# Optimization experiments

Hardware: AMD Instinct MI355X
Metric: run time of the kernel (lower is better)

## Reference

```python
import jax, jax.numpy as jnp
import numpy as np

NEG_BIG = -1e30  # safe "-inf" for masked softmax (avoids NaN for fully-masked rows)


def setup_inputs() -> dict:
    key = jax.random.key(0)
    k1, k2, k3, k4, k5, k6 = jax.random.split(key, 6)
    B, Kmax, D, C = 64, 512, 256, 1000
    deep_feats = jax.random.normal(k1, (B, D), dtype=jnp.float32)
    n = jax.random.normal(k2, (B, Kmax, D), dtype=jnp.float32)
    w = jax.random.uniform(k3, (B, Kmax), dtype=jnp.float32)
    cls_score = jax.random.normal(k4, (B, Kmax, C), dtype=jnp.float32)
    target = jax.random.randint(k5, (B,), 0, C, dtype=jnp.int64)
    lengths = jax.random.randint(k6, (B,), 1, Kmax + 1, dtype=jnp.int64)
    return {"deep_feats": deep_feats, "n": n, "w": w, "cls_score": cls_score,
            "target": target, "lengths": lengths}


def reference(deep_feats, n, w, cls_score, target, lengths):
    # deep_feats: [B,D], n: [B,Kmax,D], w: [B,Kmax], cls_score: [B,Kmax,C]
    # target: [B] int, lengths: [B] int (number of valid neighbors per sample)
    B, Kmax, C = cls_score.shape
    mask = jnp.arange(Kmax)[None, :] < lengths[:, None]          # [B,Kmax]

    # per-neighbor L2 distance ||f_i - n_ij||
    diff = deep_feats[:, None, :] - n                             # [B,Kmax,D]
    dist = jnp.sqrt(jnp.sum(diff * diff, axis=-1))                # [B,Kmax]

    s = -w * dist                                                 # [B,Kmax]
    # f_loss = sum_i -w_i . dist_i over valid neighbors
    f_loss = jnp.sum(jnp.where(mask, s, 0.0))

    # rho_i = softmax over valid neighbors of -w*dist
    logits = jnp.where(mask, s, NEG_BIG)
    rho = jax.nn.softmax(logits, axis=-1) * mask                  # [B,Kmax]

    # per-neighbor cross-entropy: -log_softmax(cls_score[b,k])[target[b]]
    logp = jax.nn.log_softmax(cls_score, axis=-1)                 # [B,Kmax,C]
    idx = jnp.broadcast_to(target[:, None, None], (B, Kmax, 1))
    ce = -jnp.take_along_axis(logp, idx, axis=-1)[..., 0]         # [B,Kmax]

    g_loss = jnp.sum(rho * ce)
    return f_loss + g_loss
```

## Files before the change

### kernel.cpp

```cpp
#include <hip/hip_runtime.h>
#include <math.h>

#define BB 64
#define KMAX 512
#define DD 256
#define CC 1000
#define NBLK1 (BB * KMAX / 4)
#define PPB 128

__device__ __forceinline__ float wave_reduce_sum(float v) {
    #pragma unroll
    for (int off = 32; off > 0; off >>= 1) v += __shfl_xor(v, off, 64);
    return v;
}

__global__ void __launch_bounds__(256)
dos_row_kernel(const float* __restrict__ deep, const float* __restrict__ n,
               const float* __restrict__ w, const float* __restrict__ cls,
               const int* __restrict__ target, const int* __restrict__ lengths,
               float* __restrict__ part_s, float* __restrict__ part_e,
               float* __restrict__ part_ec, float* __restrict__ out) {
    const int wid  = threadIdx.x >> 6;
    const int lane = threadIdx.x & 63;
    const int row  = blockIdx.x * 4 + wid;
    const int b    = row >> 9;
    const int k    = row & (KMAX - 1);
    const int len  = lengths[b];

    if (blockIdx.x == 0 && threadIdx.x == 0) out[0] = 0.f;

    if ((blockIdx.x * 4 & (KMAX - 1)) >= len) {
        if (threadIdx.x == 0) {
            part_s[blockIdx.x] = 0.f; part_e[blockIdx.x] = 0.f; part_ec[blockIdx.x] = 0.f;
        }
        return;
    }

    float sv = 0.f, ev = 0.f, ecv = 0.f;
    if (k < len) {
        const float4 dv = ((const float4*)(deep + (size_t)b * DD))[lane];
        const float4 nv = ((const float4*)(n + (size_t)row * DD))[lane];
        const float* __restrict__ x = cls + (size_t)row * CC;
        const float4 v0 = ((const float4*)x)[lane];
        const float4 v1 = ((const float4*)x)[lane + 64];
        const float4 v2 = ((const float4*)x)[lane + 128];
        float4 v3 = make_float4(-1e30f, -1e30f, -1e30f, -1e30f);
        if (lane < 58) v3 = ((const float4*)x)[lane + 192];

        const float dx = dv.x - nv.x, dy = dv.y - nv.y;
        const float dz = dv.z - nv.z, dw = dv.w - nv.w;
        float acc = dx*dx + dy*dy + dz*dz + dw*dw;
        acc = wave_reduce_sum(acc);

        float e = __expf(v0.x) + __expf(v0.y) + __expf(v0.z) + __expf(v0.w)
                + __expf(v1.x) + __expf(v1.y) + __expf(v1.z) + __expf(v1.w)
                + __expf(v2.x) + __expf(v2.y) + __expf(v2.z) + __expf(v2.w)
                + __expf(v3.x) + __expf(v3.y) + __expf(v3.z) + __expf(v3.w);
        e = wave_reduce_sum(e);

        if (lane == 0) {
            sv  = -w[row] * sqrtf(acc);
            ev  = __expf(sv);
            ecv = ev * (__logf(e) - x[target[b]]);
        }
    }

    __shared__ float red[4][3];
    if (lane == 0) { red[wid][0] = sv; red[wid][1] = ev; red[wid][2] = ecv; }
    __syncthreads();
    if (threadIdx.x == 0) {
        part_s[blockIdx.x]  = red[0][0] + red[1][0] + red[2][0] + red[3][0];
        part_e[blockIdx.x]  = red[0][1] + red[1][1] + red[2][1] + red[3][1];
        part_ec[blockIdx.x] = red[0][2] + red[1][2] + red[2][2] + red[3][2];
    }
}

__global__ void __launch_bounds__(128)
dos_final_kernel(const float* __restrict__ part_s, const float* __restrict__ part_e,
                 const float* __restrict__ part_ec, float* __restrict__ out) {
    const int b = blockIdx.x;
    const int t = threadIdx.x;
    float ss = part_s[b * PPB + t];
    float se = part_e[b * PPB + t];
    float sc = part_ec[b * PPB + t];
    ss = wave_reduce_sum(ss);
    se = wave_reduce_sum(se);
    sc = wave_reduce_sum(sc);

    __shared__ float r[2][3];
    if ((t & 63) == 0) { r[t >> 6][0] = ss; r[t >> 6][1] = se; r[t >> 6][2] = sc; }
    __syncthreads();
    if (t == 0) {
        const float S  = r[0][0] + r[1][0];
        const float E  = r[0][1] + r[1][1];
        const float EC = r[0][2] + r[1][2];
        atomicAdd(out, S + EC / E);
    }
}

extern "C" void kernel_launch(void* const* d_in, const int* in_sizes, int n_in,
                              void* d_out, int out_size, void* d_ws, size_t ws_size,
                              hipStream_t stream) {
    const float* deep    = (const float*)d_in[0];
    const float* n       = (const float*)d_in[1];
    const float* w       = (const float*)d_in[2];
    const float* cls     = (const float*)d_in[3];
    const int*   target  = (const int*)d_in[4];
    const int*   lengths = (const int*)d_in[5];
    float*       out     = (float*)d_out;

    float* ws      = (float*)d_ws;
    float* part_s  = ws;
    float* part_e  = ws + NBLK1;
    float* part_ec = ws + 2 * NBLK1;

    dos_row_kernel<<<NBLK1, 256, 0, stream>>>(deep, n, w, cls, target, lengths,
                                              part_s, part_e, part_ec, out);
    dos_final_kernel<<<BB, PPB, 0, stream>>>(part_s, part_e, part_ec, out);
}
```

Measured before the change: 22.30 us.

## Replace final reduction kernel with atomic per-sample accumulation and last-block finalize

Removes the second reduction kernel. Each block now atomically adds its partial sums into per-sample accumulators, and the last block for each sample (found with an atomic counter) computes S + EC/E and adds it to the output. A tiny init kernel zeroes the accumulators and counters. This adds four atomics per block and a small extra launch. Blocks past the valid length still run the sync and counter increment instead of returning early.

```diff
diff --git a/kernel.cpp b/kernel.cpp
--- a/kernel.cpp
+++ b/kernel.cpp
@@ -5,8 +5,8 @@
 #define KMAX 512
 #define DD 256
 #define CC 1000
-#define NBLK1 (BB * KMAX / 4)
-#define PPB 128
+#define NBLK (BB * KMAX / 4)
+#define BPB (KMAX / 4)
 
 __device__ __forceinline__ float wave_reduce_sum(float v) {
     #pragma unroll
@@ -14,27 +14,28 @@
     return v;
 }
 
+__global__ void dos_init(float* __restrict__ accS, float* __restrict__ accE,
+                         float* __restrict__ accEC, unsigned* __restrict__ cnt,
+                         float* __restrict__ out) {
+    const int t = threadIdx.x;
+    accS[t] = 0.f; accE[t] = 0.f; accEC[t] = 0.f; cnt[t] = 0u;
+    if (t == 0) out[0] = 0.f;
+}
+
 __global__ void __launch_bounds__(256)
-dos_row_kernel(const float* __restrict__ deep, const float* __restrict__ n,
-               const float* __restrict__ w, const float* __restrict__ cls,
-               const int* __restrict__ target, const int* __restrict__ lengths,
-               float* __restrict__ part_s, float* __restrict__ part_e,
-               float* __restrict__ part_ec, float* __restrict__ out) {
+dos_main(const float* __restrict__ deep, const float* __restrict__ n,
+         const float* __restrict__ w, const float* __restrict__ cls,
+         const int* __restrict__ target, const int* __restrict__ lengths,
+         float* __restrict__ accS, float* __restrict__ accE,
+         float* __restrict__ accEC, unsigned* __restrict__ cnt,
+         float* __restrict__ out) {
     const int wid  = threadIdx.x >> 6;
     const int lane = threadIdx.x & 63;
     const int row  = blockIdx.x * 4 + wid;
     const int b    = row >> 9;
     const int k    = row & (KMAX - 1);
     const int len  = lengths[b];
-
-    if (blockIdx.x == 0 && threadIdx.x == 0) out[0] = 0.f;
-
-    if ((blockIdx.x * 4 & (KMAX - 1)) >= len) {
-        if (threadIdx.x == 0) {
-            part_s[blockIdx.x] = 0.f; part_e[blockIdx.x] = 0.f; part_ec[blockIdx.x] = 0.f;
-        }
-        return;
-    }
+    const int kblk = (blockIdx.x * 4) & (KMAX - 1);
 
     float sv = 0.f, ev = 0.f, ecv = 0.f;
     if (k < len) {
@@ -68,33 +69,25 @@
     __shared__ float red[4][3];
     if (lane == 0) { red[wid][0] = sv; red[wid][1] = ev; red[wid][2] = ecv; }
     __syncthreads();
+
     if (threadIdx.x == 0) {
-        part_s[blockIdx.x]  = red[0][0] + red[1][0] + red[2][0] + red[3][0];
-        part_e[blockIdx.x]  = red[0][1] + red[1][1] + red[2][1] + red[3][1];
-        part_ec[blockIdx.x] = red[0][2] + red[1][2] + red[2][2] + red[3][2];
-    }
-}
-
-__global__ void __launch_bounds__(128)
-dos_final_kernel(const float* __restrict__ part_s, const float* __restrict__ part_e,
-                 const float* __restrict__ part_ec, float* __restrict__ out) {
-    const int b = blockIdx.x;
-    const int t = threadIdx.x;
-    float ss = part_s[b * PPB + t];
-    float se = part_e[b * PPB + t];
-    float sc = part_ec[b * PPB + t];
-    ss = wave_reduce_sum(ss);
-    se = wave_reduce_sum(se);
-    sc = wave_reduce_sum(sc);
-
-    __shared__ float r[2][3];
-    if ((t & 63) == 0) { r[t >> 6][0] = ss; r[t >> 6][1] = se; r[t >> 6][2] = sc; }
-    __syncthreads();
-    if (t == 0) {
-        const float S  = r[0][0] + r[1][0];
-        const float E  = r[0][1] + r[1][1];
-        const float EC = r[0][2] + r[1][2];
-        atomicAdd(out, S + EC / E);
+        if (kblk < len) {
+            const float S  = red[0][0] + red[1][0] + red[2][0] + red[3][0];
+            const float E  = red[0][1] + red[1][1] + red[2][1] + red[3][1];
+            const float EC = red[0][2] + red[1][2] + red[2][2] + red[3][2];
+            atomicAdd(&accS[b],  S);
+            atomicAdd(&accE[b],  E);
+            atomicAdd(&accEC[b], EC);
+        }
+        asm volatile("s_waitcnt vmcnt(0)" ::: "memory");
+        const unsigned old = __hip_atomic_fetch_add(&cnt[b], 1u, __ATOMIC_RELAXED,
+                                                    __HIP_MEMORY_SCOPE_AGENT);
+        if (old == BPB - 1) {
+            const float Sb  = atomicAdd(&accS[b],  0.0f);
+            const float Eb  = atomicAdd(&accE[b],  0.0f);
+            const float ECb = atomicAdd(&accEC[b], 0.0f);
+            atomicAdd(out, Sb + ECb / Eb);
+        }
     }
 }
 
@@ -109,12 +102,13 @@
     const int*   lengths = (const int*)d_in[5];
     float*       out     = (float*)d_out;
 
-    float* ws      = (float*)d_ws;
-    float* part_s  = ws;
-    float* part_e  = ws + NBLK1;
-    float* part_ec = ws + 2 * NBLK1;
+    float*    ws    = (float*)d_ws;
+    float*    accS  = ws;
+    float*    accE  = ws + BB;
+    float*    accEC = ws + 2 * BB;
+    unsigned* cnt   = (unsigned*)(ws + 3 * BB);
 
-    dos_row_kernel<<<NBLK1, 256, 0, stream>>>(deep, n, w, cls, target, lengths,
-                                              part_s, part_e, part_ec, out);
-    dos_final_kernel<<<BB, PPB, 0, stream>>>(part_s, part_e, part_ec, out);
+    dos_init<<<1, 64, 0, stream>>>(accS, accE, accEC, cnt, out);
+    dos_main<<<NBLK, 256, 0, stream>>>(deep, n, w, cls, target, lengths,
+                                       accS, accE, accEC, cnt, out);
 }
```

Result: slower. 69.56 us (+211.9%).
